# Performance work log

Hardware: AMD Instinct MI355X
Metric: run time of the kernel (lower is better)

Reference implementation:

```python
import jax, jax.numpy as jnp
import numpy as np

D = 1024  # d_model (all ATTENTION_CONST widths)
N = 4096  # sequence length


def setup_inputs() -> dict:
    key = jax.random.key(0)
    ks = jax.random.split(key, 11)
    s = 1.0 / np.sqrt(D)
    return {
        "q": jax.random.normal(ks[0], (N, D), jnp.float32),
        "k": jax.random.normal(ks[1], (N, D), jnp.float32),
        "v": jax.random.normal(ks[2], (N, D), jnp.float32),
        "wq_w": jax.random.normal(ks[3], (D, D), jnp.float32) * s,
        "wq_b": jax.random.normal(ks[4], (D,), jnp.float32) * s,
        "wk_w": jax.random.normal(ks[5], (D, D), jnp.float32) * s,
        "wk_b": jax.random.normal(ks[6], (D,), jnp.float32) * s,
        "wv_w": jax.random.normal(ks[7], (D, D), jnp.float32) * s,
        "wv_b": jax.random.normal(ks[8], (D,), jnp.float32) * s,
        "wo_w": jax.random.normal(ks[9], (D, D), jnp.float32) * s,
        "wo_b": jax.random.normal(ks[10], (D,), jnp.float32) * s,
    }


def reference(q, k, v, wq_w, wq_b, wk_w, wk_b, wv_w, wv_b, wo_w, wo_b):
    # Linear projections (torch convention: y = x @ W.T + b)
    qp = q @ wq_w.T + wq_b  # [N, D]
    kp = k @ wk_w.T + wk_b  # [N, D]
    vp = v @ wv_w.T + wv_b  # [N, D]
    # Naive attention: NO sqrt(d) scaling, NO head split (faithful to source)
    scores = qp @ kp.T                      # [N, N]
    attention_weights = jax.nn.softmax(scores, axis=-1)
    x = attention_weights @ vp              # [N, D]
    x = x @ wo_w.T + wo_b                   # output projection
    return (x, attention_weights)
```

## Files before the change

kernel.cpp:

```cpp
#include <hip/hip_runtime.h>
#include <cstdint>

#define N_SEQ 4096
#define DMODEL 1024

#define BM 128
#define BN 128
#define BN2 64
#define UNITE 4096

typedef __bf16 bf16_t;
typedef _Float16 f16_t;
typedef f16_t f16x8 __attribute__((ext_vector_type(8)));
typedef f16_t f16x4 __attribute__((ext_vector_type(4)));
typedef float f32x4 __attribute__((ext_vector_type(4)));

typedef __attribute__((address_space(1))) void* as1ptr;
typedef __attribute__((address_space(3))) void* as3ptr;

__device__ __forceinline__ void gload16(const void* g, void* l) {
  __builtin_amdgcn_global_load_lds((as1ptr)(uintptr_t)g, (as3ptr)(uintptr_t)l,
                                   16, 0, 0);
}

#define SBAR() asm volatile("s_barrier" ::: "memory")
#define WAITLGKM(n)                                              \
  do {                                                           \
    asm volatile("s_waitcnt lgkmcnt(" #n ")" ::: "memory");      \
    __builtin_amdgcn_sched_barrier(0);                           \
  } while (0)
#define WAITVM(n) asm volatile("s_waitcnt vmcnt(" #n ")" ::: "memory")

__global__ __launch_bounds__(256)
void qkv_proj(const f16_t* __restrict__ qh, const f16_t* __restrict__ ql,
              const f16_t* __restrict__ wq, const float* __restrict__ wq_b,
              const f16_t* __restrict__ kh, const f16_t* __restrict__ kl,
              const f16_t* __restrict__ wk, const float* __restrict__ wk_b,
              const f16_t* __restrict__ vh, const f16_t* __restrict__ wv,
              const float* __restrict__ wv_b,
              f16_t* __restrict__ QPh, f16_t* __restrict__ KPh,
              f16_t* __restrict__ VPt)
{
  __shared__ __align__(16) f16_t lds[6 * UNITE];

  const int z = blockIdx.z;
  const f16_t *A0, *A1 = nullptr, *B0;
  const float* bias;
  if (z == 0)      { A0 = qh; A1 = ql; B0 = wq; bias = wq_b; }
  else if (z == 1) { A0 = kh; A1 = kl; B0 = wk; bias = wk_b; }
  else             { A0 = vh;          B0 = wv; bias = wv_b; }
  const bool twop = (z < 2);

  const int M = N_SEQ, Nc = DMODEL, K = DMODEL;
  const int t = threadIdx.x;
  const int lane = t & 63;
  const int wave = t >> 6;
  const int wm = wave >> 1;
  const int wn = wave & 1;

  const int gx = gridDim.x;
  const int nwg = gx * gridDim.y;
  const int flat = blockIdx.y * gx + blockIdx.x;
  const int swz = (flat & 7) * (nwg >> 3) + (flat >> 3);
  const int row0 = (swz / gx) * BM;
  const int col0 = (swz % gx) * BN;

  const int srw = t >> 3;
  const int scol = 8 * ((t & 7) ^ ((t >> 3) & 7));
  const int sdst = t * 8;

  const int fr = lane & 15;
  const int kq = (lane >> 4) * 8;
  const int sw = (fr & 7) << 3;

  f32x4 acc[4][4] = {};

  for (int k0 = 0; k0 < K; k0 += 64) {
#pragma unroll
    for (int h = 0; h < 2; ++h) {
      const int r = h * 32 + srw;
      gload16(A0 + (size_t)(row0 + r) * K + k0 + scol,
              &lds[0 * UNITE + h * 2048 + sdst]);
      gload16(A0 + (size_t)(row0 + 64 + r) * K + k0 + scol,
              &lds[1 * UNITE + h * 2048 + sdst]);
      gload16(B0 + (size_t)(col0 + r) * K + k0 + scol,
              &lds[4 * UNITE + h * 2048 + sdst]);
      gload16(B0 + (size_t)(col0 + 64 + r) * K + k0 + scol,
              &lds[5 * UNITE + h * 2048 + sdst]);
      if (twop) {
        gload16(A1 + (size_t)(row0 + r) * K + k0 + scol,
                &lds[2 * UNITE + h * 2048 + sdst]);
        gload16(A1 + (size_t)(row0 + 64 + r) * K + k0 + scol,
                &lds[3 * UNITE + h * 2048 + sdst]);
      }
    }
    __syncthreads();

    f16x8 ah[4][2], al[4][2], bh[4][2];
#pragma unroll
    for (int m = 0; m < 4; ++m) {
      const int r = (m * 16 + fr) * 64;
#pragma unroll
      for (int ks = 0; ks < 2; ++ks) {
        const int c = (ks * 32 + kq) ^ sw;
        ah[m][ks] = *(const f16x8*)&lds[wm * UNITE + r + c];
        if (twop) al[m][ks] = *(const f16x8*)&lds[(2 + wm) * UNITE + r + c];
      }
    }
#pragma unroll
    for (int n = 0; n < 4; ++n) {
      const int r = (n * 16 + fr) * 64;
#pragma unroll
      for (int ks = 0; ks < 2; ++ks)
        bh[n][ks] = *(const f16x8*)&lds[(4 + wn) * UNITE + r +
                                        (((ks * 32 + kq)) ^ sw)];
    }

#pragma unroll
    for (int m = 0; m < 4; ++m)
#pragma unroll
      for (int n = 0; n < 4; ++n)
#pragma unroll
        for (int ks = 0; ks < 2; ++ks) {
          acc[m][n] = __builtin_amdgcn_mfma_f32_16x16x32_f16(
              ah[m][ks], bh[n][ks], acc[m][n], 0, 0, 0);
          if (twop)
            acc[m][n] = __builtin_amdgcn_mfma_f32_16x16x32_f16(
                al[m][ks], bh[n][ks], acc[m][n], 0, 0, 0);
        }
    __syncthreads();
  }

#pragma unroll
  for (int m = 0; m < 4; ++m) {
#pragma unroll
    for (int n = 0; n < 4; ++n) {
      const int grow0 = row0 + wm * 64 + m * 16 + (lane >> 4) * 4;
      const int gcol = col0 + wn * 64 + n * 16 + (lane & 15);
      const float bv = bias[gcol];
      if (z == 2) {
        f16x4 p;
#pragma unroll
        for (int r = 0; r < 4; ++r) p[r] = (f16_t)(acc[m][n][r] + bv);
        *(f16x4*)&VPt[(size_t)gcol * M + grow0] = p;
      } else {
        f16_t* out = (z == 0) ? QPh : KPh;
#pragma unroll
        for (int r = 0; r < 4; ++r)
          out[(size_t)(grow0 + r) * Nc + gcol] = (f16_t)(acc[m][n][r] + bv);
      }
    }
  }
}

template <int OUT_F32>
__global__ __launch_bounds__(256)
void gemm_f16p(const f16_t* __restrict__ A, const f16_t* __restrict__ B,
               const float* __restrict__ bias,
               f16_t* __restrict__ Cf16, float* __restrict__ Cf32,
               int M, int Nc, int K)
{
  __shared__ __align__(16) f16_t lds[2 * 3 * UNITE];

  const int gx = gridDim.x;
  const int nwg = gx * gridDim.y;
  const int flat = blockIdx.y * gx + blockIdx.x;
  const int swz = (flat & 7) * (nwg >> 3) + (flat >> 3);
  const int bx = swz % gx;
  const int by = swz / gx;

  const int t = threadIdx.x;
  const int lane = t & 63;
  const int wave = t >> 6;
  const int wm = wave >> 1;
  const int wn = wave & 1;
  const int row0 = by * BM;
  const int col0 = bx * BN2;

  const int srw = t >> 3;
  const int scol = 8 * ((t & 7) ^ ((t >> 3) & 7));
  const int sdst = t * 8;

  const int fr = lane & 15;
  const int kq = (lane >> 4) * 8;
  const int sw = (fr & 7) << 3;

  auto stage = [&](int buf, int kt) {
    const int k0 = kt << 6;
#pragma unroll
    for (int h = 0; h < 2; ++h) {
      const int r = h * 32 + srw;
      gload16(A + (size_t)(row0 + r) * K + k0 + scol,
              &lds[(buf * 3 + 0) * UNITE + h * 2048 + sdst]);
      gload16(A + (size_t)(row0 + 64 + r) * K + k0 + scol,
              &lds[(buf * 3 + 1) * UNITE + h * 2048 + sdst]);
      gload16(B + (size_t)(col0 + r) * K + k0 + scol,
              &lds[(buf * 3 + 2) * UNITE + h * 2048 + sdst]);
    }
  };

  f32x4 acc[4][2] = {};
  const int NT = K >> 6;

  stage(0, 0);
  stage(1, 1);
  WAITVM(6);
  SBAR();

  for (int kt = 0; kt < NT; ++kt) {
    const int p = kt & 1;
    const f16_t* Ab = &lds[(p * 3 + wm) * UNITE];
    const f16_t* Bb = &lds[(p * 3 + 2) * UNITE];

    f16x8 ah[4][2], bh[2][2];
#pragma unroll
    for (int m = 0; m < 2; ++m)
#pragma unroll
      for (int ks = 0; ks < 2; ++ks)
        ah[m][ks] = *(const f16x8*)&Ab[(m * 16 + fr) * 64 +
                                       ((ks * 32 + kq) ^ sw)];
#pragma unroll
    for (int n = 0; n < 2; ++n)
#pragma unroll
      for (int ks = 0; ks < 2; ++ks)
        bh[n][ks] = *(const f16x8*)&Bb[(wn * 32 + n * 16 + fr) * 64 +
                                       ((ks * 32 + kq) ^ sw)];
#pragma unroll
    for (int m = 2; m < 4; ++m)
#pragma unroll
      for (int ks = 0; ks < 2; ++ks)
        ah[m][ks] = *(const f16x8*)&Ab[(m * 16 + fr) * 64 +
                                       ((ks * 32 + kq) ^ sw)];

    WAITLGKM(4);
#pragma unroll
    for (int m = 0; m < 2; ++m)
#pragma unroll
      for (int n = 0; n < 2; ++n)
#pragma unroll
        for (int ks = 0; ks < 2; ++ks)
          acc[m][n] = __builtin_amdgcn_mfma_f32_16x16x32_f16(
              ah[m][ks], bh[n][ks], acc[m][n], 0, 0, 0);
    WAITLGKM(0);
#pragma unroll
    for (int m = 2; m < 4; ++m)
#pragma unroll
      for (int n = 0; n < 2; ++n)
#pragma unroll
        for (int ks = 0; ks < 2; ++ks)
          acc[m][n] = __builtin_amdgcn_mfma_f32_16x16x32_f16(
              ah[m][ks], bh[n][ks], acc[m][n], 0, 0, 0);

    SBAR();
    if (kt + 2 < NT) {
      stage(p, kt + 2);
      WAITVM(6);
    } else if (kt + 1 < NT) {
      WAITVM(0);
    }
    SBAR();
  }

#pragma unroll
  for (int m = 0; m < 4; ++m) {
#pragma unroll
    for (int n = 0; n < 2; ++n) {
      const int grow0 = row0 + wm * 64 + m * 16 + (lane >> 4) * 4;
      const int gcol = col0 + wn * 32 + n * 16 + (lane & 15);
#pragma unroll
      for (int r = 0; r < 4; ++r) {
        const size_t idx = (size_t)(grow0 + r) * Nc + gcol;
        if (OUT_F32) Cf32[idx] = acc[m][n][r] + bias[gcol];
        else         Cf16[idx] = (f16_t)acc[m][n][r];
      }
    }
  }
}

#define TILE_ELEMS 16384
#define UNIT_ELEMS 4096
#define NT_SC 16

template <int V> struct ic { static constexpr int value = V; };

template <int MH>
__device__ __forceinline__ void load_A8f(const f16_t* Ab, int wm, int fr,
                                         int kq, int sw, f16x8 (&af)[4][2]) {
#pragma unroll
  for (int m = 0; m < 4; ++m) {
    const int row = wm * 128 + (MH * 4 + m) * 16 + fr;
#pragma unroll
    for (int ks = 0; ks < 2; ++ks)
      af[m][ks] = *(const f16x8*)&Ab[row * 64 + ((ks * 32 + kq) ^ sw)];
  }
}

template <int NH>
__device__ __forceinline__ void load_B4f(const f16_t* Bb, int wn, int fr,
                                         int kq, int sw, f16x8 (&bfr)[2][2]) {
#pragma unroll
  for (int n = 0; n < 2; ++n) {
    const int row = wn * 64 + (NH * 2 + n) * 16 + fr;
#pragma unroll
    for (int ks = 0; ks < 2; ++ks)
      bfr[n][ks] = *(const f16x8*)&Bb[row * 64 + ((ks * 32 + kq) ^ sw)];
  }
}

template <int MH, int NH>
__device__ __forceinline__ void mfma16f(const f16x8 (&af)[4][2],
                                        const f16x8 (&bfr)[2][2],
                                        f32x4 (&acc)[8][4]) {
#pragma unroll
  for (int m = 0; m < 4; ++m)
#pragma unroll
    for (int n = 0; n < 2; ++n)
#pragma unroll
      for (int ks = 0; ks < 2; ++ks)
        acc[MH * 4 + m][NH * 2 + n] = __builtin_amdgcn_mfma_f32_16x16x32_f16(
            af[m][ks], bfr[n][ks], acc[MH * 4 + m][NH * 2 + n], 0, 0, 0);
}

__global__ __launch_bounds__(512, 1)
void gemm8f_scores(const f16_t* __restrict__ Qh, const f16_t* __restrict__ Kh,
                   float* __restrict__ C)
{
  __shared__ __align__(16) f16_t sm[2 * 2 * TILE_ELEMS];

  const int t = threadIdx.x;
  const int lane = t & 63;
  const int wave = t >> 6;
  const int wm = wave >> 2;
  const int wn = wave & 3;

  const int flat = blockIdx.y * 16 + blockIdx.x;
  const int swzb = (flat & 7) * 32 + (flat >> 3);
  const int brow = (swzb >> 4) * 256;
  const int bcol = (swzb & 15) * 256;

  const int srow = t >> 3;
  const int scol = 8 * ((t & 7) ^ ((t >> 3) & 7));
  const int sdst = t * 8;

  const int fr = lane & 15;
  const int kq = (lane >> 4) * 8;
  const int sw = (fr & 7) << 3;

  auto stageA = [&](int buf, int u, int kt) {
    const int kk = kt << 6;
    gload16(Qh + (size_t)(brow + u * 64 + srow) * DMODEL + kk + scol,
            &sm[(buf * 2 + 0) * TILE_ELEMS + u * UNIT_ELEMS + sdst]);
  };
  auto stageB = [&](int buf, int u, int kt) {
    const int kk = kt << 6;
    gload16(Kh + (size_t)(bcol + u * 64 + srow) * DMODEL + kk + scol,
            &sm[(buf * 2 + 1) * TILE_ELEMS + u * UNIT_ELEMS + sdst]);
  };

  f32x4 acc[8][4] = {};
  f16x8 af0[4][2], af1[4][2];
  f16x8 b0[2][2], b1[2][2];

#pragma unroll
  for (int u = 0; u < 4; ++u) stageA(0, u, 0);
#pragma unroll
  for (int u = 0; u < 4; ++u) stageB(0, u, 0);
  stageA(1, 0, 1); stageA(1, 2, 1);
  stageB(1, 0, 1); stageB(1, 1, 1);
  stageA(1, 1, 1); stageA(1, 3, 1);
  WAITVM(6);
  SBAR();

  auto tile = [&](auto Pc, int kt) {
    constexpr int p = decltype(Pc)::value;
    constexpr int q = p ^ 1;
    const bool n1 = (kt + 1 < NT_SC);
    const bool n2 = (kt + 2 < NT_SC);
    const f16_t* Ab = &sm[(p * 2 + 0) * TILE_ELEMS];
    const f16_t* Bb = &sm[(p * 2 + 1) * TILE_ELEMS];

    load_A8f<0>(Ab, wm, fr, kq, sw, af0);
    load_B4f<0>(Bb, wn, fr, kq, sw, b0);
    if (n1) { stageB(q, 2, kt + 1); stageB(q, 3, kt + 1); }
    load_B4f<1>(Bb, wn, fr, kq, sw, b1);
    WAITLGKM(4);
    __builtin_amdgcn_s_setprio(1);
    mfma16f<0, 0>(af0, b0, acc);
    __builtin_amdgcn_s_setprio(0);
    __builtin_amdgcn_sched_barrier(0);
    SBAR();

    if (n2) { stageA(p, 0, kt + 2); stageA(p, 2, kt + 2); }
    load_A8f<1>(Ab, wm, fr, kq, sw, af1);
    WAITLGKM(8);
    __builtin_amdgcn_s_setprio(1);
    mfma16f<0, 1>(af0, b1, acc);
    __builtin_amdgcn_s_setprio(0);
    __builtin_amdgcn_sched_barrier(0);
    SBAR();

    if (n2) { stageB(p, 0, kt + 2); stageB(p, 1, kt + 2); }
    WAITLGKM(0);
    __builtin_amdgcn_s_setprio(1);
    mfma16f<1, 0>(af1, b0, acc);
    __builtin_amdgcn_s_setprio(0);
    __builtin_amdgcn_sched_barrier(0);
    SBAR();

    if (n2) { stageA(p, 1, kt + 2); stageA(p, 3, kt + 2); }
    __builtin_amdgcn_s_setprio(1);
    mfma16f<1, 1>(af1, b1, acc);
    __builtin_amdgcn_s_setprio(0);
    __builtin_amdgcn_sched_barrier(0);
    if (n2)      WAITVM(6);
    else if (n1) WAITVM(0);
    SBAR();
  };

  for (int kt = 0; kt < NT_SC; kt += 2) {
    tile(ic<0>{}, kt);
    tile(ic<1>{}, kt + 1);
  }

#pragma unroll
  for (int mf = 0; mf < 8; ++mf) {
#pragma unroll
    for (int nf = 0; nf < 4; ++nf) {
      const int r0 = brow + wm * 128 + mf * 16 + (lane >> 4) * 4;
      const int c  = bcol + wn * 64 + nf * 16 + (lane & 15);
#pragma unroll
      for (int r = 0; r < 4; ++r)
        C[(size_t)(r0 + r) * N_SEQ + c] = acc[mf][nf][r];
    }
  }
}

struct SplitDesc {
  const float* src[7];
  f16_t* hi[7];
  f16_t* lo[7];
  int mode[7];
  int blk_start[8];
};

__global__ __launch_bounds__(256)
void split_all(SplitDesc d)
{
  const int b = blockIdx.x;
  int seg = 0;
#pragma unroll
  for (int s = 1; s < 7; ++s) seg += (b >= d.blk_start[s]) ? 1 : 0;
  const int i = (b - d.blk_start[seg]) * 256 + threadIdx.x;
  const float4 v = ((const float4*)d.src[seg])[i];
  const float vv[4] = {v.x, v.y, v.z, v.w};
  f16x4 h, l;
#pragma unroll
  for (int j = 0; j < 4; ++j) {
    const f16_t hh = (f16_t)vv[j];
    h[j] = hh;
    l[j] = (f16_t)(vv[j] - (float)hh);
  }
  ((f16x4*)d.hi[seg])[i] = h;
  if (d.mode[seg] == 2) ((f16x4*)d.lo[seg])[i] = l;
}

__global__ __launch_bounds__(256)
void softmax_rows(float* __restrict__ S, f16_t* __restrict__ P, int n)
{
  const int row = blockIdx.x;
  float* srow = S + (size_t)row * n;
  f16_t* prow = P + (size_t)row * n;
  const int t = threadIdx.x;
  const int lane = t & 63;
  const int wave = t >> 6;
  __shared__ float red[8];

  float4 v[4];
  float mx = -3.4e38f;
#pragma unroll
  for (int i = 0; i < 4; ++i) {
    v[i] = *(const float4*)(srow + (size_t)(i * 256 + t) * 4);
    mx = fmaxf(mx, fmaxf(fmaxf(v[i].x, v[i].y), fmaxf(v[i].z, v[i].w)));
  }
#pragma unroll
  for (int off = 32; off > 0; off >>= 1) mx = fmaxf(mx, __shfl_xor(mx, off));
  if (lane == 0) red[wave] = mx;
  __syncthreads();
  mx = fmaxf(fmaxf(red[0], red[1]), fmaxf(red[2], red[3]));

  float e[16];
  float sum = 0.f;
#pragma unroll
  for (int i = 0; i < 4; ++i) {
    e[4 * i + 0] = __expf(v[i].x - mx);
    e[4 * i + 1] = __expf(v[i].y - mx);
    e[4 * i + 2] = __expf(v[i].z - mx);
    e[4 * i + 3] = __expf(v[i].w - mx);
    sum += e[4 * i + 0] + e[4 * i + 1] + e[4 * i + 2] + e[4 * i + 3];
  }
#pragma unroll
  for (int off = 32; off > 0; off >>= 1) sum += __shfl_xor(sum, off);
  if (lane == 0) red[4 + wave] = sum;
  __syncthreads();
  sum = red[4] + red[5] + red[6] + red[7];
  const float inv = 1.0f / sum;

#pragma unroll
  for (int i = 0; i < 4; ++i) {
    float4 w;
    w.x = e[4 * i + 0] * inv;
    w.y = e[4 * i + 1] * inv;
    w.z = e[4 * i + 2] * inv;
    w.w = e[4 * i + 3] * inv;
    *(float4*)(srow + (size_t)(i * 256 + t) * 4) = w;
    f16x4 p;
    p[0] = (f16_t)w.x;
    p[1] = (f16_t)w.y;
    p[2] = (f16_t)w.z;
    p[3] = (f16_t)w.w;
    *(f16x4*)(prow + (size_t)(i * 256 + t) * 4) = p;
  }
}

extern "C" void kernel_launch(void* const* d_in, const int* in_sizes, int n_in,
                              void* d_out, int out_size, void* d_ws, size_t ws_size,
                              hipStream_t stream) {
  const int N = N_SEQ, D = DMODEL;
  const float* q    = (const float*)d_in[0];
  const float* k    = (const float*)d_in[1];
  const float* v    = (const float*)d_in[2];
  const float* wq_w = (const float*)d_in[3];
  const float* wq_b = (const float*)d_in[4];
  const float* wk_w = (const float*)d_in[5];
  const float* wk_b = (const float*)d_in[6];
  const float* wv_w = (const float*)d_in[7];
  const float* wv_b = (const float*)d_in[8];
  const float* wo_w = (const float*)d_in[9];
  const float* wo_b = (const float*)d_in[10];

  float* x_out = (float*)d_out;
  float* attn  = x_out + (size_t)N * D;

  char* wsp = (char*)d_ws;
  auto alloc = [&](size_t bytes) { char* p = wsp; wsp += bytes; return p; };
  const size_t ND = (size_t)N * D, DD = (size_t)D * D;
  f16_t*  qh16  = (f16_t*)alloc(ND * 2);
  f16_t*  ql16  = (f16_t*)alloc(ND * 2);
  f16_t*  kh16  = (f16_t*)alloc(ND * 2);
  f16_t*  kl16  = (f16_t*)alloc(ND * 2);
  f16_t*  vh16  = (f16_t*)alloc(ND * 2);
  f16_t*  wq16  = (f16_t*)alloc(DD * 2);
  f16_t*  wk16  = (f16_t*)alloc(DD * 2);
  f16_t*  wv16  = (f16_t*)alloc(DD * 2);
  f16_t*  wo16  = (f16_t*)alloc(DD * 2);
  f16_t*  QPh   = (f16_t*)alloc(ND * 2);
  f16_t*  pad1  = (f16_t*)alloc(ND * 2);
  f16_t*  KPh   = (f16_t*)alloc(ND * 2);
  f16_t*  pad2  = (f16_t*)alloc(ND * 2);
  f16_t*  VPt   = (f16_t*)alloc(ND * 2);
  f16_t*  Pb    = QPh;
  f16_t*  Xb    = vh16;
  (void)pad1; (void)pad2;

  SplitDesc sd;
  sd.src[0] = q;    sd.hi[0] = qh16;  sd.lo[0] = ql16;    sd.mode[0] = 2;
  sd.src[1] = k;    sd.hi[1] = kh16;  sd.lo[1] = kl16;    sd.mode[1] = 2;
  sd.src[2] = v;    sd.hi[2] = vh16;  sd.lo[2] = nullptr; sd.mode[2] = 3;
  sd.src[3] = wq_w; sd.hi[3] = wq16;  sd.lo[3] = nullptr; sd.mode[3] = 3;
  sd.src[4] = wk_w; sd.hi[4] = wk16;  sd.lo[4] = nullptr; sd.mode[4] = 3;
  sd.src[5] = wv_w; sd.hi[5] = wv16;  sd.lo[5] = nullptr; sd.mode[5] = 3;
  sd.src[6] = wo_w; sd.hi[6] = wo16;  sd.lo[6] = nullptr; sd.mode[6] = 3;
  const int nb_nd = (int)(ND / 4 / 256);
  const int nb_dd = (int)(DD / 4 / 256);
  sd.blk_start[0] = 0;
  sd.blk_start[1] = nb_nd;
  sd.blk_start[2] = 2 * nb_nd;
  sd.blk_start[3] = 3 * nb_nd;
  sd.blk_start[4] = 3 * nb_nd + nb_dd;
  sd.blk_start[5] = 3 * nb_nd + 2 * nb_dd;
  sd.blk_start[6] = 3 * nb_nd + 3 * nb_dd;
  sd.blk_start[7] = 3 * nb_nd + 4 * nb_dd;
  split_all<<<dim3(sd.blk_start[7]), dim3(256), 0, stream>>>(sd);

  const dim3 blk(256);
  const dim3 gsc(N / 256, N / 256);
  const dim3 gd(D / BN2, N / BM);

  qkv_proj<<<dim3(D / BN, N / BM, 3), blk, 0, stream>>>(
      qh16, ql16, wq16, wq_b,
      kh16, kl16, wk16, wk_b,
      vh16, wv16, wv_b,
      QPh, KPh, VPt);

  gemm8f_scores<<<gsc, dim3(512), 0, stream>>>(QPh, KPh, attn);

  softmax_rows<<<dim3(N), blk, 0, stream>>>(attn, Pb, N);

  gemm_f16p<0><<<gd, blk, 0, stream>>>(
      Pb, VPt, nullptr, Xb, nullptr, N, D, N);

  gemm_f16p<1><<<gd, blk, 0, stream>>>(
      Xb, wo16, wo_b, nullptr, x_out, N, D, D);
}
```

Measured before the change: 209.1 us.

## Replace 256x256 8-wave scores GEMM with simpler 128x128 4-wave double-buffered kernel

Swaps the hand-scheduled 256x256 tile, 512-thread scores GEMM (interleaved LDS loads, setprio, sched barriers) for a generic 128x128 tile, 256-thread kernel with plain double buffering. The grid becomes 32x32 workgroups with a grouped swizzle. This gives more workgroups and lower register/LDS pressure per block, which could improve occupancy and load balance. In exchange it loses data reuse per tile and the fine-grained overlap of loads with MFMA work.

Result: faster. 196.2 us (median of 3 runs) (-6.2%).

```diff
diff --git a/kernel.cpp b/kernel.cpp
--- a/kernel.cpp
+++ b/kernel.cpp
@@ -277,68 +277,28 @@
   }
 }
 
-#define TILE_ELEMS 16384
-#define UNIT_ELEMS 4096
-#define NT_SC 16
-
-template <int V> struct ic { static constexpr int value = V; };
-
-template <int MH>
-__device__ __forceinline__ void load_A8f(const f16_t* Ab, int wm, int fr,
-                                         int kq, int sw, f16x8 (&af)[4][2]) {
-#pragma unroll
-  for (int m = 0; m < 4; ++m) {
-    const int row = wm * 128 + (MH * 4 + m) * 16 + fr;
-#pragma unroll
-    for (int ks = 0; ks < 2; ++ks)
-      af[m][ks] = *(const f16x8*)&Ab[row * 64 + ((ks * 32 + kq) ^ sw)];
-  }
-}
-
-template <int NH>
-__device__ __forceinline__ void load_B4f(const f16_t* Bb, int wn, int fr,
-                                         int kq, int sw, f16x8 (&bfr)[2][2]) {
-#pragma unroll
-  for (int n = 0; n < 2; ++n) {
-    const int row = wn * 64 + (NH * 2 + n) * 16 + fr;
-#pragma unroll
-    for (int ks = 0; ks < 2; ++ks)
-      bfr[n][ks] = *(const f16x8*)&Bb[row * 64 + ((ks * 32 + kq) ^ sw)];
-  }
-}
-
-template <int MH, int NH>
-__device__ __forceinline__ void mfma16f(const f16x8 (&af)[4][2],
-                                        const f16x8 (&bfr)[2][2],
-                                        f32x4 (&acc)[8][4]) {
-#pragma unroll
-  for (int m = 0; m < 4; ++m)
-#pragma unroll
-    for (int n = 0; n < 2; ++n)
-#pragma unroll
-      for (int ks = 0; ks < 2; ++ks)
-        acc[MH * 4 + m][NH * 2 + n] = __builtin_amdgcn_mfma_f32_16x16x32_f16(
-            af[m][ks], bfr[n][ks], acc[MH * 4 + m][NH * 2 + n], 0, 0, 0);
-}
-
-__global__ __launch_bounds__(512, 1)
-void gemm8f_scores(const f16_t* __restrict__ Qh, const f16_t* __restrict__ Kh,
-                   float* __restrict__ C)
+__global__ __launch_bounds__(256)
+void gemm_f16s(const f16_t* __restrict__ A, const f16_t* __restrict__ B,
+               float* __restrict__ C, int M, int Nc, int K)
 {
-  __shared__ __align__(16) f16_t sm[2 * 2 * TILE_ELEMS];
+  __shared__ __align__(16) f16_t lds[2 * 4 * UNITE];
+
+  const int gx = gridDim.x;
+  const int nwg = gx * gridDim.y;
+  const int flat = blockIdx.y * gx + blockIdx.x;
+  const int swz = (flat & 7) * (nwg >> 3) + (flat >> 3);
+  const int bx = swz % gx;
+  const int by = swz / gx;
 
   const int t = threadIdx.x;
   const int lane = t & 63;
   const int wave = t >> 6;
-  const int wm = wave >> 2;
-  const int wn = wave & 3;
-
-  const int flat = blockIdx.y * 16 + blockIdx.x;
-  const int swzb = (flat & 7) * 32 + (flat >> 3);
-  const int brow = (swzb >> 4) * 256;
-  const int bcol = (swzb & 15) * 256;
-
-  const int srow = t >> 3;
+  const int wm = wave >> 1;
+  const int wn = wave & 1;
+  const int row0 = by * BM;
+  const int col0 = bx * BN;
+
+  const int srw = t >> 3;
   const int scol = 8 * ((t & 7) ^ ((t >> 3) & 7));
   const int sdst = t * 8;
 
@@ -346,91 +306,93 @@
   const int kq = (lane >> 4) * 8;
   const int sw = (fr & 7) << 3;
 
-  auto stageA = [&](int buf, int u, int kt) {
-    const int kk = kt << 6;
-    gload16(Qh + (size_t)(brow + u * 64 + srow) * DMODEL + kk + scol,
-            &sm[(buf * 2 + 0) * TILE_ELEMS + u * UNIT_ELEMS + sdst]);
+  auto stage = [&](int buf, int kt) {
+    const int k0 = kt << 6;
+#pragma unroll
+    for (int h = 0; h < 2; ++h) {
+      const int r = h * 32 + srw;
+      gload16(A + (size_t)(row0 + r) * K + k0 + scol,
+              &lds[(buf * 4 + 0) * UNITE + h * 2048 + sdst]);
+      gload16(A + (size_t)(row0 + 64 + r) * K + k0 + scol,
+              &lds[(buf * 4 + 1) * UNITE + h * 2048 + sdst]);
+      gload16(B + (size_t)(col0 + r) * K + k0 + scol,
+              &lds[(buf * 4 + 2) * UNITE + h * 2048 + sdst]);
+      gload16(B + (size_t)(col0 + 64 + r) * K + k0 + scol,
+              &lds[(buf * 4 + 3) * UNITE + h * 2048 + sdst]);
+    }
   };
-  auto stageB = [&](int buf, int u, int kt) {
-    const int kk = kt << 6;
-    gload16(Kh + (size_t)(bcol + u * 64 + srow) * DMODEL + kk + scol,
-            &sm[(buf * 2 + 1) * TILE_ELEMS + u * UNIT_ELEMS + sdst]);
-  };
-
-  f32x4 acc[8][4] = {};
-  f16x8 af0[4][2], af1[4][2];
-  f16x8 b0[2][2], b1[2][2];
-
-#pragma unroll
-  for (int u = 0; u < 4; ++u) stageA(0, u, 0);
-#pragma unroll
-  for (int u = 0; u < 4; ++u) stageB(0, u, 0);
-  stageA(1, 0, 1); stageA(1, 2, 1);
-  stageB(1, 0, 1); stageB(1, 1, 1);
-  stageA(1, 1, 1); stageA(1, 3, 1);
-  WAITVM(6);
+
+  f32x4 acc[4][4] = {};
+  const int NT = K >> 6;
+
+  stage(0, 0);
+  stage(1, 1);
+  WAITVM(8);
   SBAR();
 
-  auto tile = [&](auto Pc, int kt) {
-    constexpr int p = decltype(Pc)::value;
-    constexpr int q = p ^ 1;
-    const bool n1 = (kt + 1 < NT_SC);
-    const bool n2 = (kt + 2 < NT_SC);
-    const f16_t* Ab = &sm[(p * 2 + 0) * TILE_ELEMS];
-    const f16_t* Bb = &sm[(p * 2 + 1) * TILE_ELEMS];
-
-    load_A8f<0>(Ab, wm, fr, kq, sw, af0);
-    load_B4f<0>(Bb, wn, fr, kq, sw, b0);
-    if (n1) { stageB(q, 2, kt + 1); stageB(q, 3, kt + 1); }
-    load_B4f<1>(Bb, wn, fr, kq, sw, b1);
+  for (int kt = 0; kt < NT; ++kt) {
+    const int p = kt & 1;
+    const f16_t* Ab = &lds[(p * 4 + wm) * UNITE];
+    const f16_t* Bb = &lds[(p * 4 + 2 + wn) * UNITE];
+
+    f16x8 ah[4][2], bh[4][2];
+#pragma unroll
+    for (int m = 0; m < 4; ++m)
+#pragma unroll
+      for (int ks = 0; ks < 2; ++ks)
+        ah[m][ks] = *(const f16x8*)&Ab[(m * 16 + fr) * 64 +
+                                       ((ks * 32 + kq) ^ sw)];
+#pragma unroll
+    for (int n = 0; n < 2; ++n)
+#pragma unroll
+      for (int ks = 0; ks < 2; ++ks)
+        bh[n][ks] = *(const f16x8*)&Bb[(n * 16 + fr) * 64 +
+                                       ((ks * 32 + kq) ^ sw)];
+#pragma unroll
+    for (int n = 2; n < 4; ++n)
+#pragma unroll
+      for (int ks = 0; ks < 2; ++ks)
+        bh[n][ks] = *(const f16x8*)&Bb[(n * 16 + fr) * 64 +
+                                       ((ks * 32 + kq) ^ sw)];
+
     WAITLGKM(4);
-    __builtin_amdgcn_s_setprio(1);
-    mfma16f<0, 0>(af0, b0, acc);
-    __builtin_amdgcn_s_setprio(0);
-    __builtin_amdgcn_sched_barrier(0);
+#pragma unroll
+    for (int m = 0; m < 4; ++m)
+#pragma unroll
+      for (int n = 0; n < 2; ++n)
+#pragma unroll
+        for (int ks = 0; ks < 2; ++ks)
+          acc[m][n] = __builtin_amdgcn_mfma_f32_16x16x32_f16(
+              ah[m][ks], bh[n][ks], acc[m][n], 0, 0, 0);
+    WAITLGKM(0);
+#pragma unroll
+    for (int m = 0; m < 4; ++m)
+#pragma unroll
+      for (int n = 2; n < 4; ++n)
+#pragma unroll
+        for (int ks = 0; ks < 2; ++ks)
+          acc[m][n] = __builtin_amdgcn_mfma_f32_16x16x32_f16(
+              ah[m][ks], bh[n][ks], acc[m][n], 0, 0, 0);
+
     SBAR();
-
-    if (n2) { stageA(p, 0, kt + 2); stageA(p, 2, kt + 2); }
-    load_A8f<1>(Ab, wm, fr, kq, sw, af1);
-    WAITLGKM(8);
-    __builtin_amdgcn_s_setprio(1);
-    mfma16f<0, 1>(af0, b1, acc);
-    __builtin_amdgcn_s_setprio(0);
-    __builtin_amdgcn_sched_barrier(0);
+    if (kt + 2 < NT) {
+      stage(p, kt + 2);
+      WAITVM(8);
+    } else if (kt + 1 < NT) {
+      WAITVM(0);
+    }
     SBAR();
-
-    if (n2) { stageB(p, 0, kt + 2); stageB(p, 1, kt + 2); }
-    WAITLGKM(0);
-    __builtin_amdgcn_s_setprio(1);
-    mfma16f<1, 0>(af1, b0, acc);
-    __builtin_amdgcn_s_setprio(0);
-    __builtin_amdgcn_sched_barrier(0);
-    SBAR();
-
-    if (n2) { stageA(p, 1, kt + 2); stageA(p, 3, kt + 2); }
-    __builtin_amdgcn_s_setprio(1);
-    mfma16f<1, 1>(af1, b1, acc);
-    __builtin_amdgcn_s_setprio(0);
-    __builtin_amdgcn_sched_barrier(0);
-    if (n2)      WAITVM(6);
-    else if (n1) WAITVM(0);
-    SBAR();
-  };
-
-  for (int kt = 0; kt < NT_SC; kt += 2) {
-    tile(ic<0>{}, kt);
-    tile(ic<1>{}, kt + 1);
-  }
-
-#pragma unroll
-  for (int mf = 0; mf < 8; ++mf) {
-#pragma unroll
-    for (int nf = 0; nf < 4; ++nf) {
-      const int r0 = brow + wm * 128 + mf * 16 + (lane >> 4) * 4;
-      const int c  = bcol + wn * 64 + nf * 16 + (lane & 15);
+  }
+
+#pragma unroll
+  for (int m = 0; m < 4; ++m) {
+#pragma unroll
+    for (int n = 0; n < 4; ++n) {
+      const int grow0 = row0 + wm * 64 + m * 16 + (lane >> 4) * 4;
+      const int gcol = col0 + wn * 64 + n * 16 + (lane & 15);
 #pragma unroll
       for (int r = 0; r < 4; ++r)
-        C[(size_t)(r0 + r) * N_SEQ + c] = acc[mf][nf][r];
+        C[(size_t)(grow0 + r) * Nc + gcol] = acc[m][n][r];
     }
   }
 }
@@ -583,7 +545,7 @@
   split_all<<<dim3(sd.blk_start[7]), dim3(256), 0, stream>>>(sd);
 
   const dim3 blk(256);
-  const dim3 gsc(N / 256, N / 256);
+  const dim3 gsc(N / BN, N / BM);
   const dim3 gd(D / BN2, N / BM);
 
   qkv_proj<<<dim3(D / BN, N / BM, 3), blk, 0, stream>>>(
@@ -592,7 +554,7 @@
       vh16, wv16, wv_b,
       QPh, KPh, VPt);
 
-  gemm8f_scores<<<gsc, dim3(512), 0, stream>>>(QPh, KPh, attn);
+  gemm_f16s<<<gsc, blk, 0, stream>>>(QPh, KPh, attn, N, N, D);
 
   softmax_rows<<<dim3(N), blk, 0, stream>>>(attn, Pb, N);
 
```
